# Kernel optimization log

Measured on AMD Instinct MI355X. Metric: run time of the kernel, lower is better.

The kernel has to match this reference:

```python
import jax, jax.numpy as jnp
import numpy as np

B, S, D = 8, 2048, 512


def setup_inputs() -> dict:
    key = jax.random.key(0)
    ks = jax.random.split(key, 8)
    x = jax.random.normal(ks[0], (B, S, D), dtype=jnp.float32)
    mask = jax.random.randint(ks[1], (B, S, 1), 0, 2, dtype=jnp.int32)
    Wq = jax.random.normal(ks[2], (D, D), dtype=jnp.float32) / np.sqrt(D)
    bq = jax.random.normal(ks[3], (D,), dtype=jnp.float32) * 0.01
    Wk = jax.random.normal(ks[4], (D, D), dtype=jnp.float32) / np.sqrt(D)
    bk = jax.random.normal(ks[5], (D,), dtype=jnp.float32) * 0.01
    Wv = jax.random.normal(ks[6], (D, D), dtype=jnp.float32) / np.sqrt(D)
    bv = jax.random.normal(ks[7], (D,), dtype=jnp.float32) * 0.01
    return {"x": x, "mask": mask, "Wq": Wq, "bq": bq, "Wk": Wk, "bk": bk, "Wv": Wv, "bv": bv}


def reference(x, mask, Wq, bq, Wk, bk, Wv, bv):
    # torch Linear: y = x @ W^T + b
    Q = jnp.einsum('bsd,ed->bse', x, Wq) + bq
    K = jnp.einsum('bsd,ed->bse', x, Wk) + bk
    V = jnp.einsum('bsd,ed->bse', x, Wv) + bv
    scale = 1.0 / jnp.sqrt(jnp.asarray(x.shape[-1], dtype=x.dtype))
    scores = jnp.einsum('bqd,bkd->bqk', Q, K) * scale  # [B, S, S]
    attn_mask = jnp.transpose(mask, (0, 2, 1))  # [B, 1, S], broadcasts over queries
    scores = jnp.where(attn_mask == 0, jnp.asarray(-10000.0, dtype=scores.dtype), scores)
    attn = jax.nn.softmax(scores, axis=-1)
    return jnp.einsum('bqk,bkd->bqd', attn, V)
```

## Files before the change

### kernel.cpp

```cpp
#include <hip/hip_runtime.h>
#include <cstddef>

#define BB 8
#define SS 2048
#define DD 512
#define MM (BB * SS)

typedef __attribute__((ext_vector_type(8))) short bf16x8;
typedef __attribute__((ext_vector_type(4))) float f32x4;
typedef __attribute__((ext_vector_type(4))) unsigned short u16x4;

__device__ __forceinline__ f32x4 mfma16(bf16x8 a, bf16x8 b, f32x4 c) {
  return __builtin_amdgcn_mfma_f32_16x16x32_bf16(a, b, c, 0, 0, 0);
}
__device__ __forceinline__ unsigned short f2bf(float f) {
  unsigned int u = __float_as_uint(f);
  u += 0x7fffu + ((u >> 16) & 1u);
  return (unsigned short)(u >> 16);
}
__device__ __forceinline__ void gld16(const void* g, void* l) {
  __builtin_amdgcn_global_load_lds((const __attribute__((address_space(1))) void*)g,
                                   (__attribute__((address_space(3))) void*)l, 16, 0, 0);
}

__global__ void cvt_bf16_kernel(const float* __restrict__ in,
                                unsigned short* __restrict__ out, int n4) {
  int i = blockIdx.x * blockDim.x + threadIdx.x;
  if (i >= n4) return;
  f32x4 v = reinterpret_cast<const f32x4*>(in)[i];
  u16x4 o;
  o[0] = f2bf(v[0]);
  o[1] = f2bf(v[1]);
  o[2] = f2bf(v[2]);
  o[3] = f2bf(v[3]);
  reinterpret_cast<u16x4*>(out)[i] = o;
}
__global__ void cvt_w3_kernel(const float* __restrict__ s0, const float* __restrict__ s1,
                              const float* __restrict__ s2, unsigned short* __restrict__ d0,
                              unsigned short* __restrict__ d1, unsigned short* __restrict__ d2) {
  const float* s = blockIdx.y == 0 ? s0 : (blockIdx.y == 1 ? s1 : s2);
  unsigned short* d = blockIdx.y == 0 ? d0 : (blockIdx.y == 1 ? d1 : d2);
  int i = blockIdx.x * blockDim.x + threadIdx.x;
  f32x4 v = reinterpret_cast<const f32x4*>(s)[i];
  u16x4 o;
  o[0] = f2bf(v[0]);
  o[1] = f2bf(v[1]);
  o[2] = f2bf(v[2]);
  o[3] = f2bf(v[3]);
  reinterpret_cast<u16x4*>(d)[i] = o;
}

__global__ void mask_scan_kernel(const int* __restrict__ mask, int* __restrict__ idx,
                                 int* __restrict__ nbArr) {
  __shared__ int part[256];
  const int b = blockIdx.x;
  const int t = threadIdx.x;
  int m[8], c = 0;
#pragma unroll
  for (int e = 0; e < 8; ++e) {
    m[e] = mask[b * SS + t * 8 + e];
    c += (m[e] != 0);
  }
  int v = c;
  part[t] = v;
  __syncthreads();
  for (int off = 1; off < 256; off <<= 1) {
    int u = (t >= off) ? part[t - off] : 0;
    __syncthreads();
    v += u;
    part[t] = v;
    __syncthreads();
  }
  int base = v - c;
#pragma unroll
  for (int e = 0; e < 8; ++e)
    if (m[e]) idx[b * SS + base++] = t * 8 + e;
  const int nb = part[255];
  if (t == 255) nbArr[b] = nb;
  for (int j = nb + t; j < SS; j += 256) idx[b * SS + j] = 0;
}

__global__ __launch_bounds__(256, 2) void qkv_gemm_kernel(
    const unsigned short* __restrict__ X, const unsigned short* __restrict__ W0,
    const unsigned short* __restrict__ W1, const unsigned short* __restrict__ W2,
    const float* __restrict__ b0, const float* __restrict__ b1,
    const float* __restrict__ b2, unsigned short* __restrict__ O0,
    unsigned short* __restrict__ O1, unsigned short* __restrict__ O2) {
  __shared__ unsigned char a_lds[128 * 128];
  __shared__ unsigned char b_lds[128 * 128];
  const int tid = threadIdx.x;
  const int w = tid >> 6, l = tid & 63, lr = l & 15, hi = l >> 4;
  const int which = blockIdx.y >> 2;
  const unsigned short* W = which == 0 ? W0 : (which == 1 ? W1 : W2);
  const float* bias = which == 0 ? b0 : (which == 1 ? b1 : b2);
  unsigned short* out = which == 0 ? O0 : (which == 1 ? O1 : O2);
  const int m0 = blockIdx.x * 128;
  const int n0 = (blockIdx.y & 3) * 128;
  const int wm = (w >> 1) * 64, wn = (w & 1) * 64;
  const int srow = l >> 3, gchunk = (l & 7) ^ (srow & 7);

  f32x4 acc[4][4];
#pragma unroll
  for (int mt = 0; mt < 4; ++mt)
#pragma unroll
    for (int nt = 0; nt < 4; ++nt) acc[mt][nt] = (f32x4){0.f, 0.f, 0.f, 0.f};

  const unsigned short* ga = X + (size_t)(m0 + w * 32 + srow) * DD + gchunk * 8;
  const unsigned short* gb = W + (size_t)(n0 + w * 32 + srow) * DD + gchunk * 8;

  for (int k0 = 0; k0 < DD; k0 += 64) {
#pragma unroll
    for (int ii = 0; ii < 4; ++ii) {
      gld16(ga + (size_t)ii * 8 * DD + k0, &a_lds[(w * 4 + ii) * 1024]);
      gld16(gb + (size_t)ii * 8 * DD + k0, &b_lds[(w * 4 + ii) * 1024]);
    }
    __syncthreads();
#pragma unroll
    for (int dkl = 0; dkl < 2; ++dkl) {
      const int gc = dkl * 4 + hi;
      bf16x8 af[4], bfr[4];
#pragma unroll
      for (int mt = 0; mt < 4; ++mt) {
        const int row = wm + mt * 16 + lr;
        af[mt] = *reinterpret_cast<const bf16x8*>(
            &a_lds[row * 128 + ((gc ^ (row & 7)) * 16)]);
      }
#pragma unroll
      for (int nt = 0; nt < 4; ++nt) {
        const int row = wn + nt * 16 + lr;
        bfr[nt] = *reinterpret_cast<const bf16x8*>(
            &b_lds[row * 128 + ((gc ^ (row & 7)) * 16)]);
      }
#pragma unroll
      for (int mt = 0; mt < 4; ++mt)
#pragma unroll
        for (int nt = 0; nt < 4; ++nt)
          acc[mt][nt] = mfma16(af[mt], bfr[nt], acc[mt][nt]);
    }
    __syncthreads();
  }

#pragma unroll
  for (int nt = 0; nt < 4; ++nt) {
    const int col = n0 + wn + nt * 16 + lr;
    const float bv = bias[col];
#pragma unroll
    for (int mt = 0; mt < 4; ++mt)
#pragma unroll
      for (int r = 0; r < 4; ++r) {
        const int row = m0 + wm + mt * 16 + hi * 4 + r;
        out[(size_t)row * DD + col] = f2bf(acc[mt][nt][r] + bv);
      }
  }
}

__global__ void vtrans_kernel(const unsigned short* __restrict__ V,
                              const int* __restrict__ idx, const int* __restrict__ nbArr,
                              unsigned short* __restrict__ VT2) {
  __shared__ unsigned short t[64][72];
  const int b = blockIdx.z;
  const int kt = blockIdx.x;
  const int d0 = blockIdx.y * 64;
  const int tid = threadIdx.x;
  const int c = tid & 63, rg = tid >> 6;
  const int nb = nbArr[b];
#pragma unroll
  for (int i = 0; i < 16; ++i) {
    const int row = rg * 16 + i;
    const int s = kt * 64 + row;
    const int src = s < nb ? idx[b * SS + s] : 0;
    t[row][c] = V[((size_t)b * SS + src) * DD + d0 + c];
  }
  __syncthreads();
#pragma unroll
  for (int i = 0; i < 16; ++i) {
    const int ix = i * 256 + tid;
    const int jj = ix & 7;
    const int dl = (ix >> 3) & 63;
    const int cc = ix >> 9;
    VT2[(((size_t)(b * 32 + kt) * 8 + cc) * 512 + d0 + dl) * 8 + jj] =
        t[cc * 8 + jj][dl];
  }
}

__global__ __launch_bounds__(256, 2) void attn_kernel(
    const unsigned short* __restrict__ Q, const unsigned short* __restrict__ K,
    const unsigned short* __restrict__ VT2, const int* __restrict__ idx,
    const int* __restrict__ nbArr, float* __restrict__ Out,
    float* __restrict__ Apart, float* __restrict__ mlpart) {
  __shared__ unsigned char k_lds[32 * 1024];
  __shared__ unsigned char vt_lds[4 * 512 * 16];
  __shared__ unsigned short pbuf[4][16][32];
  const int tid = threadIdx.x;
  const int w = tid >> 6, l = tid & 63, lr = l & 15, hi = l >> 4;
  const int bid = blockIdx.x;
  const int b = bid & 7;
  const int qt = (bid >> 3) >> 1;
  const int sp = (bid >> 3) & 1;
  const int q0 = qt * 64 + w * 16;
  const float scale = 0.044194173824159216f;

  const int nb = nbArr[b];
  const int ntile = (nb + 31) >> 5;
  const int half = (ntile + 1) >> 1;
  const int lo = sp == 0 ? 0 : half;
  const int hi_t = sp == 0 ? half : ntile;

  const unsigned short* __restrict__ Qb = Q + (size_t)b * SS * DD;
  const unsigned short* __restrict__ Kb = K + (size_t)b * SS * DD;
  const unsigned short* __restrict__ Vb = VT2 + (size_t)b * SS * DD;
  const int* __restrict__ idxb = idx + b * SS;

  bf16x8 qf[16];
#pragma unroll
  for (int dk = 0; dk < 16; ++dk)
    qf[dk] = *reinterpret_cast<const bf16x8*>(
        &Qb[(size_t)(q0 + lr) * DD + dk * 32 + hi * 8]);

  f32x4 oacc[32];
#pragma unroll
  for (int i = 0; i < 32; ++i) oacc[i] = (f32x4){0.f, 0.f, 0.f, 0.f};
  float mrow[4], lrow[4];
#pragma unroll
  for (int r = 0; r < 4; ++r) {
    mrow[r] = -10000.0f;
    lrow[r] = 0.0f;
  }

  for (int t = lo; t < hi_t; ++t) {
#pragma unroll
    for (int r = 0; r < 8; ++r) {
      const int row = w * 8 + r;
      const int j = t * 32 + row;
      const int src = idxb[j];
      const int ch = (l & 56) | ((l ^ row) & 7);
      gld16(Kb + (size_t)src * DD + ch * 8, &k_lds[row * 1024]);
    }
    const size_t vbase = ((size_t)((t >> 1) * 8 + (t & 1) * 4 + w) * 512);
#pragma unroll
    for (int g = 0; g < 8; ++g)
      gld16(Vb + (vbase + g * 64 + l) * 8, &vt_lds[(w * 512 + g * 64) * 16]);
    __syncthreads();

    f32x4 sacc[2];
#pragma unroll
    for (int nt = 0; nt < 2; ++nt) sacc[nt] = (f32x4){0.f, 0.f, 0.f, 0.f};
#pragma unroll
    for (int dk = 0; dk < 16; ++dk) {
#pragma unroll
      for (int nt = 0; nt < 2; ++nt) {
        const int row = nt * 16 + lr;
        const int c = dk * 4 + hi;
        bf16x8 bk = *reinterpret_cast<const bf16x8*>(
            &k_lds[row * 1024 + ((c & ~7) | ((c ^ row) & 7)) * 16]);
        sacc[nt] = mfma16(qf[dk], bk, sacc[nt]);
      }
    }

    float s[2][4];
#pragma unroll
    for (int nt = 0; nt < 2; ++nt) {
      const int j = t * 32 + nt * 16 + lr;
      const bool ok = j < nb;
#pragma unroll
      for (int r = 0; r < 4; ++r)
        s[nt][r] = ok ? sacc[nt][r] * scale : -10000.0f;
    }

    float mnew[4], alpha[4];
#pragma unroll
    for (int r = 0; r < 4; ++r) {
      float mx = fmaxf(s[0][r], s[1][r]);
#pragma unroll
      for (int off = 1; off < 16; off <<= 1) mx = fmaxf(mx, __shfl_xor(mx, off));
      mnew[r] = fmaxf(mrow[r], mx);
      alpha[r] = __expf(mrow[r] - mnew[r]);
      mrow[r] = mnew[r];
    }
    float rs[4] = {0.f, 0.f, 0.f, 0.f};
#pragma unroll
    for (int nt = 0; nt < 2; ++nt)
#pragma unroll
      for (int r = 0; r < 4; ++r) {
        float p = __expf(s[nt][r] - mnew[r]);
        s[nt][r] = p;
        rs[r] += p;
      }
#pragma unroll
    for (int r = 0; r < 4; ++r) {
      float tt = rs[r];
#pragma unroll
      for (int off = 1; off < 16; off <<= 1) tt += __shfl_xor(tt, off);
      lrow[r] = lrow[r] * alpha[r] + tt;
    }

#pragma unroll
    for (int nt = 0; nt < 2; ++nt)
#pragma unroll
      for (int r = 0; r < 4; ++r)
        pbuf[w][hi * 4 + r][nt * 16 + lr] = f2bf(s[nt][r]);
    bf16x8 pf = *reinterpret_cast<const bf16x8*>(&pbuf[w][lr][hi * 8]);

    const float aprod = alpha[0] * alpha[1] * alpha[2] * alpha[3];
    unsigned long long bal = __ballot(aprod == 1.0f);
    if (bal != ~0ull) {
#pragma unroll
      for (int nt2 = 0; nt2 < 32; ++nt2)
#pragma unroll
        for (int r = 0; r < 4; ++r) oacc[nt2][r] *= alpha[r];
    }
#pragma unroll
    for (int nt2 = 0; nt2 < 32; ++nt2) {
      bf16x8 v0 = *reinterpret_cast<const bf16x8*>(
          &vt_lds[(hi * 512 + nt2 * 16 + lr) * 16]);
      oacc[nt2] = mfma16(pf, v0, oacc[nt2]);
    }
    __syncthreads();
  }

  float* Ap = sp == 0 ? Out : Apart;
#pragma unroll
  for (int nt2 = 0; nt2 < 32; ++nt2)
#pragma unroll
    for (int r = 0; r < 4; ++r)
      Ap[((size_t)b * SS + q0 + hi * 4 + r) * DD + nt2 * 16 + lr] = oacc[nt2][r];
  if (lr == 0) {
#pragma unroll
    for (int r = 0; r < 4; ++r) {
      const size_t row = (size_t)sp * MM + b * SS + q0 + hi * 4 + r;
      mlpart[row * 2 + 0] = mrow[r];
      mlpart[row * 2 + 1] = lrow[r];
    }
  }
}

__global__ void combine_kernel(float* __restrict__ Out, const float* __restrict__ Apart,
                               const float* __restrict__ mlpart) {
  const int gid = blockIdx.x * 256 + threadIdx.x;
  const int row = gid >> 7;
  const float m1 = mlpart[(size_t)row * 2 + 0];
  const float l1 = mlpart[(size_t)row * 2 + 1];
  const float m2 = mlpart[((size_t)MM + row) * 2 + 0];
  const float l2 = mlpart[((size_t)MM + row) * 2 + 1];
  const float m = fmaxf(m1, m2);
  const float w1 = __expf(m1 - m), w2 = __expf(m2 - m);
  const float inv = 1.0f / (w1 * l1 + w2 * l2);
  f32x4 a1 = reinterpret_cast<f32x4*>(Out)[gid];
  f32x4 a2 = reinterpret_cast<const f32x4*>(Apart)[gid];
  f32x4 o;
#pragma unroll
  for (int e = 0; e < 4; ++e) o[e] = (w1 * a1[e] + w2 * a2[e]) * inv;
  reinterpret_cast<f32x4*>(Out)[gid] = o;
}

extern "C" void kernel_launch(void* const* d_in, const int* in_sizes, int n_in,
                              void* d_out, int out_size, void* d_ws, size_t ws_size,
                              hipStream_t stream) {
  const float* x = (const float*)d_in[0];
  const int* mask = (const int*)d_in[1];
  const float* Wq = (const float*)d_in[2];
  const float* bq = (const float*)d_in[3];
  const float* Wk = (const float*)d_in[4];
  const float* bk = (const float*)d_in[5];
  const float* Wv = (const float*)d_in[6];
  const float* bv = (const float*)d_in[7];
  float* out = (float*)d_out;

  char* ws = (char*)d_ws;
  const size_t MB = 1024 * 1024;
  unsigned short* Qb = (unsigned short*)(ws);
  unsigned short* Kb = (unsigned short*)(ws + 16 * MB);
  unsigned short* VT2b = (unsigned short*)(ws + 32 * MB);
  unsigned short* Xb = (unsigned short*)(ws + 48 * MB);
  unsigned short* Vb = (unsigned short*)(ws + 64 * MB);
  float* Apart = (float*)(ws + 48 * MB);
  unsigned short* Wqb = (unsigned short*)(ws + 80 * MB);
  unsigned short* Wkb = Wqb + 512 * 512;
  unsigned short* Wvb = Wkb + 512 * 512;
  int* idx = (int*)(ws + 82 * MB);
  int* nbArr = (int*)(ws + 82 * MB + 65536);
  float* mlpart = (float*)(ws + 82 * MB + 128 * 1024);

  cvt_bf16_kernel<<<8192, 256, 0, stream>>>(x, Xb, (MM * DD) / 4);
  cvt_w3_kernel<<<dim3(256, 3), 256, 0, stream>>>(Wq, Wk, Wv, Wqb, Wkb, Wvb);
  mask_scan_kernel<<<BB, 256, 0, stream>>>(mask, idx, nbArr);

  qkv_gemm_kernel<<<dim3(MM / 128, 12), 256, 0, stream>>>(
      Xb, Wqb, Wkb, Wvb, bq, bk, bv, Qb, Kb, Vb);

  vtrans_kernel<<<dim3(SS / 64, DD / 64, BB), 256, 0, stream>>>(Vb, idx, nbArr, VT2b);

  attn_kernel<<<512, 256, 0, stream>>>(Qb, Kb, VT2b, idx, nbArr, out, Apart, mlpart);

  combine_kernel<<<(MM * DD / 4) / 256, 256, 0, stream>>>(out, Apart, mlpart);
}
```

Before: 252.5 us.

## Double-buffer K/V tiles in attention and use 8-wave blocks over 128 queries

The attention kernel now prefetches the next K and V tile into a second LDS buffer while computing on the current one, and waits with a raw vmcnt/barrier at the end of each iteration. Blocks grow to 512 threads covering 128 queries, so each K/V tile is shared by twice as many waves and the per-wave load share is halved. This is meant to hide global-to-LDS latency and cut redundant K/V traffic. In exchange it doubles LDS use (about 80 KB per block) and halves the grid to 256 blocks, which may reduce occupancy on a device with 256 CUs.

Result: slower. 268.0 us (+6.1%).

```diff
diff --git a/kernel.cpp b/kernel.cpp
--- a/kernel.cpp
+++ b/kernel.cpp
@@ -183,21 +183,22 @@
   }
 }
 
-__global__ __launch_bounds__(256, 2) void attn_kernel(
+__global__ __launch_bounds__(512, 2) void attn_kernel(
     const unsigned short* __restrict__ Q, const unsigned short* __restrict__ K,
     const unsigned short* __restrict__ VT2, const int* __restrict__ idx,
     const int* __restrict__ nbArr, float* __restrict__ Out,
     float* __restrict__ Apart, float* __restrict__ mlpart) {
-  __shared__ unsigned char k_lds[32 * 1024];
-  __shared__ unsigned char vt_lds[4 * 512 * 16];
-  __shared__ unsigned short pbuf[4][16][32];
+  __shared__ unsigned char k_lds[2][32 * 1024];
+  __shared__ unsigned char vt_lds[2][4 * 512 * 16];
+  __shared__ unsigned short pbuf[8][16][32];
   const int tid = threadIdx.x;
   const int w = tid >> 6, l = tid & 63, lr = l & 15, hi = l >> 4;
   const int bid = blockIdx.x;
   const int b = bid & 7;
-  const int qt = (bid >> 3) >> 1;
-  const int sp = (bid >> 3) & 1;
-  const int q0 = qt * 64 + w * 16;
+  const int rest = bid >> 3;
+  const int qt = rest >> 1;
+  const int sp = rest & 1;
+  const int q0 = qt * 128 + w * 16;
   const float scale = 0.044194173824159216f;
 
   const int nb = nbArr[b];
@@ -227,20 +228,31 @@
     lrow[r] = 0.0f;
   }
 
+  auto stage = [&](int t, int buf) {
+#pragma unroll
+    for (int r = 0; r < 4; ++r) {
+      const int row = w * 4 + r;
+      const int src = idxb[t * 32 + row];
+      const int ch = (l & 56) | ((l ^ row) & 7);
+      gld16(Kb + (size_t)src * DD + ch * 8, &k_lds[buf][row * 1024]);
+    }
+    const int c2 = w >> 1;
+    const size_t vbase = ((size_t)((t >> 1) * 8 + (t & 1) * 4 + c2) * 512);
+#pragma unroll
+    for (int gg = 0; gg < 4; ++gg) {
+      const int g = (w & 1) * 4 + gg;
+      gld16(Vb + (vbase + (size_t)g * 64 + l) * 8, &vt_lds[buf][(c2 * 512 + g * 64) * 16]);
+    }
+  };
+
+  int cur = 0;
+  if (lo < hi_t) {
+    stage(lo, 0);
+    asm volatile("s_waitcnt vmcnt(0)\n\ts_barrier" ::: "memory");
+  }
+
   for (int t = lo; t < hi_t; ++t) {
-#pragma unroll
-    for (int r = 0; r < 8; ++r) {
-      const int row = w * 8 + r;
-      const int j = t * 32 + row;
-      const int src = idxb[j];
-      const int ch = (l & 56) | ((l ^ row) & 7);
-      gld16(Kb + (size_t)src * DD + ch * 8, &k_lds[row * 1024]);
-    }
-    const size_t vbase = ((size_t)((t >> 1) * 8 + (t & 1) * 4 + w) * 512);
-#pragma unroll
-    for (int g = 0; g < 8; ++g)
-      gld16(Vb + (vbase + g * 64 + l) * 8, &vt_lds[(w * 512 + g * 64) * 16]);
-    __syncthreads();
+    if (t + 1 < hi_t) stage(t + 1, cur ^ 1);
 
     f32x4 sacc[2];
 #pragma unroll
@@ -252,7 +264,7 @@
         const int row = nt * 16 + lr;
         const int c = dk * 4 + hi;
         bf16x8 bk = *reinterpret_cast<const bf16x8*>(
-            &k_lds[row * 1024 + ((c & ~7) | ((c ^ row) & 7)) * 16]);
+            &k_lds[cur][row * 1024 + ((c & ~7) | ((c ^ row) & 7)) * 16]);
         sacc[nt] = mfma16(qf[dk], bk, sacc[nt]);
       }
     }
@@ -312,10 +324,12 @@
 #pragma unroll
     for (int nt2 = 0; nt2 < 32; ++nt2) {
       bf16x8 v0 = *reinterpret_cast<const bf16x8*>(
-          &vt_lds[(hi * 512 + nt2 * 16 + lr) * 16]);
+          &vt_lds[cur][(hi * 512 + nt2 * 16 + lr) * 16]);
       oacc[nt2] = mfma16(pf, v0, oacc[nt2]);
     }
-    __syncthreads();
+
+    asm volatile("s_waitcnt vmcnt(0)\n\ts_barrier" ::: "memory");
+    cur ^= 1;
   }
 
   float* Ap = sp == 0 ? Out : Apart;
@@ -390,7 +404,7 @@
 
   vtrans_kernel<<<dim3(SS / 64, DD / 64, BB), 256, 0, stream>>>(Vb, idx, nbArr, VT2b);
 
-  attn_kernel<<<512, 256, 0, stream>>>(Qb, Kb, VT2b, idx, nbArr, out, Apart, mlpart);
+  attn_kernel<<<256, 512, 0, stream>>>(Qb, Kb, VT2b, idx, nbArr, out, Apart, mlpart);
 
   combine_kernel<<<(MM * DD / 4) / 256, 256, 0, stream>>>(out, Apart, mlpart);
 }
```

## Double-buffer K tiles, read V from global, lazy softmax rescale

Applied to the files above, without the earlier changes.

The attention kernel now double-buffers K tiles in LDS so the next tile's gather overlaps the current tile's compute. V fragments are loaded directly from global memory into registers instead of being staged through LDS. The gather indices are cached in shared memory once per block. Online-softmax rescaling only happens when the running max grows by more than a threshold, and the softmax scale is folded into the Q projection epilogue. The trade-off is that V reads lose LDS reuse and each wave now pays global-load latency for them.

Result: slower. 287.9 us (+14.0%).

```diff
diff --git a/kernel.cpp b/kernel.cpp
--- a/kernel.cpp
+++ b/kernel.cpp
@@ -94,6 +94,7 @@
   const unsigned short* W = which == 0 ? W0 : (which == 1 ? W1 : W2);
   const float* bias = which == 0 ? b0 : (which == 1 ? b1 : b2);
   unsigned short* out = which == 0 ? O0 : (which == 1 ? O1 : O2);
+  const float oscale = which == 0 ? 0.044194173824159216f : 1.0f;
   const int m0 = blockIdx.x * 128;
   const int n0 = (blockIdx.y & 3) * 128;
   const int wm = (w >> 1) * 64, wn = (w & 1) * 64;
@@ -149,7 +150,7 @@
 #pragma unroll
       for (int r = 0; r < 4; ++r) {
         const int row = m0 + wm + mt * 16 + hi * 4 + r;
-        out[(size_t)row * DD + col] = f2bf(acc[mt][nt][r] + bv);
+        out[(size_t)row * DD + col] = f2bf((acc[mt][nt][r] + bv) * oscale);
       }
   }
 }
@@ -188,9 +189,9 @@
     const unsigned short* __restrict__ VT2, const int* __restrict__ idx,
     const int* __restrict__ nbArr, float* __restrict__ Out,
     float* __restrict__ Apart, float* __restrict__ mlpart) {
-  __shared__ unsigned char k_lds[32 * 1024];
-  __shared__ unsigned char vt_lds[4 * 512 * 16];
+  __shared__ unsigned char k_lds[2][32 * 1024];
   __shared__ unsigned short pbuf[4][16][32];
+  __shared__ int ids[1024];
   const int tid = threadIdx.x;
   const int w = tid >> 6, l = tid & 63, lr = l & 15, hi = l >> 4;
   const int bid = blockIdx.x;
@@ -198,19 +199,21 @@
   const int qt = (bid >> 3) >> 1;
   const int sp = (bid >> 3) & 1;
   const int q0 = qt * 64 + w * 16;
-  const float scale = 0.044194173824159216f;
 
   const int nb = nbArr[b];
   const int ntile = (nb + 31) >> 5;
   const int half = (ntile + 1) >> 1;
   const int lo = sp == 0 ? 0 : half;
   const int hi_t = sp == 0 ? half : ntile;
+  const int ntl = hi_t - lo;
 
   const unsigned short* __restrict__ Qb = Q + (size_t)b * SS * DD;
   const unsigned short* __restrict__ Kb = K + (size_t)b * SS * DD;
   const unsigned short* __restrict__ Vb = VT2 + (size_t)b * SS * DD;
   const int* __restrict__ idxb = idx + b * SS;
 
+  for (int j = tid; j < ntl * 32; j += 256) ids[j] = idxb[lo * 32 + j];
+
   bf16x8 qf[16];
 #pragma unroll
   for (int dk = 0; dk < 16; ++dk)
@@ -227,20 +230,26 @@
     lrow[r] = 0.0f;
   }
 
-  for (int t = lo; t < hi_t; ++t) {
+  auto stage = [&](int tr, int buf) {
 #pragma unroll
     for (int r = 0; r < 8; ++r) {
       const int row = w * 8 + r;
-      const int j = t * 32 + row;
-      const int src = idxb[j];
+      const int src = ids[tr * 32 + row];
       const int ch = (l & 56) | ((l ^ row) & 7);
-      gld16(Kb + (size_t)src * DD + ch * 8, &k_lds[row * 1024]);
-    }
-    const size_t vbase = ((size_t)((t >> 1) * 8 + (t & 1) * 4 + w) * 512);
-#pragma unroll
-    for (int g = 0; g < 8; ++g)
-      gld16(Vb + (vbase + g * 64 + l) * 8, &vt_lds[(w * 512 + g * 64) * 16]);
-    __syncthreads();
+      gld16(Kb + (size_t)src * DD + ch * 8, &k_lds[buf][row * 1024]);
+    }
+  };
+
+  __syncthreads();
+  int cur = 0;
+  if (ntl > 0) {
+    stage(0, 0);
+    asm volatile("s_waitcnt vmcnt(0)" ::: "memory");
+    __builtin_amdgcn_s_barrier();
+  }
+
+  for (int t = lo; t < hi_t; ++t) {
+    if (t + 1 < hi_t) stage(t + 1 - lo, cur ^ 1);
 
     f32x4 sacc[2];
 #pragma unroll
@@ -252,7 +261,7 @@
         const int row = nt * 16 + lr;
         const int c = dk * 4 + hi;
         bf16x8 bk = *reinterpret_cast<const bf16x8*>(
-            &k_lds[row * 1024 + ((c & ~7) | ((c ^ row) & 7)) * 16]);
+            &k_lds[cur][row * 1024 + ((c & ~7) | ((c ^ row) & 7)) * 16]);
         sacc[nt] = mfma16(qf[dk], bk, sacc[nt]);
       }
     }
@@ -264,25 +273,36 @@
       const bool ok = j < nb;
 #pragma unroll
       for (int r = 0; r < 4; ++r)
-        s[nt][r] = ok ? sacc[nt][r] * scale : -10000.0f;
-    }
-
-    float mnew[4], alpha[4];
+        s[nt][r] = ok ? sacc[nt][r] : -10000.0f;
+    }
+
+    float mx[4];
+    float need = -1e30f;
 #pragma unroll
     for (int r = 0; r < 4; ++r) {
-      float mx = fmaxf(s[0][r], s[1][r]);
-#pragma unroll
-      for (int off = 1; off < 16; off <<= 1) mx = fmaxf(mx, __shfl_xor(mx, off));
-      mnew[r] = fmaxf(mrow[r], mx);
-      alpha[r] = __expf(mrow[r] - mnew[r]);
-      mrow[r] = mnew[r];
+      float m2 = fmaxf(s[0][r], s[1][r]);
+#pragma unroll
+      for (int off = 1; off < 16; off <<= 1) m2 = fmaxf(m2, __shfl_xor(m2, off));
+      mx[r] = m2;
+      need = fmaxf(need, m2 - mrow[r]);
+    }
+    if (__any(need > 8.0f)) {
+#pragma unroll
+      for (int r = 0; r < 4; ++r) {
+        const float mnew = fmaxf(mrow[r], mx[r]);
+        const float alpha = __expf(mrow[r] - mnew);
+        mrow[r] = mnew;
+        lrow[r] *= alpha;
+#pragma unroll
+        for (int nt2 = 0; nt2 < 32; ++nt2) oacc[nt2][r] *= alpha;
+      }
     }
     float rs[4] = {0.f, 0.f, 0.f, 0.f};
 #pragma unroll
     for (int nt = 0; nt < 2; ++nt)
 #pragma unroll
       for (int r = 0; r < 4; ++r) {
-        float p = __expf(s[nt][r] - mnew[r]);
+        float p = __expf(s[nt][r] - mrow[r]);
         s[nt][r] = p;
         rs[r] += p;
       }
@@ -291,7 +311,7 @@
       float tt = rs[r];
 #pragma unroll
       for (int off = 1; off < 16; off <<= 1) tt += __shfl_xor(tt, off);
-      lrow[r] = lrow[r] * alpha[r] + tt;
+      lrow[r] += tt;
     }
 
 #pragma unroll
@@ -301,21 +321,23 @@
         pbuf[w][hi * 4 + r][nt * 16 + lr] = f2bf(s[nt][r]);
     bf16x8 pf = *reinterpret_cast<const bf16x8*>(&pbuf[w][lr][hi * 8]);
 
-    const float aprod = alpha[0] * alpha[1] * alpha[2] * alpha[3];
-    unsigned long long bal = __ballot(aprod == 1.0f);
-    if (bal != ~0ull) {
-#pragma unroll
-      for (int nt2 = 0; nt2 < 32; ++nt2)
-#pragma unroll
-        for (int r = 0; r < 4; ++r) oacc[nt2][r] *= alpha[r];
-    }
-#pragma unroll
-    for (int nt2 = 0; nt2 < 32; ++nt2) {
-      bf16x8 v0 = *reinterpret_cast<const bf16x8*>(
-          &vt_lds[(hi * 512 + nt2 * 16 + lr) * 16]);
-      oacc[nt2] = mfma16(pf, v0, oacc[nt2]);
-    }
-    __syncthreads();
+    const unsigned short* vtb =
+        Vb + (((size_t)(t >> 1) * 8 + (t & 1) * 4 + hi) * 512) * 8;
+#pragma unroll
+    for (int g = 0; g < 4; ++g) {
+      bf16x8 vv[8];
+#pragma unroll
+      for (int u = 0; u < 8; ++u)
+        vv[u] = *reinterpret_cast<const bf16x8*>(
+            &vtb[(size_t)((g * 8 + u) * 16 + lr) * 8]);
+#pragma unroll
+      for (int u = 0; u < 8; ++u)
+        oacc[g * 8 + u] = mfma16(pf, vv[u], oacc[g * 8 + u]);
+    }
+
+    asm volatile("s_waitcnt vmcnt(0)" ::: "memory");
+    __builtin_amdgcn_s_barrier();
+    cur ^= 1;
   }
 
   float* Ap = sp == 0 ? Out : Apart;
```
